# Performance work log

Hardware: AMD Instinct MI355X
Metric: run time of the kernel (lower is better)

The kernel has to match this reference:

```python
import jax, jax.numpy as jnp
import numpy as np

N = 100000   # nodes
E = 1600000  # edges (before self loops)
IN, HID, HEADS, OUT = 128, 32, 2, 32


def setup_inputs() -> dict:
    key = jax.random.key(0)
    ks = jax.random.split(key, 10)
    def glorot(k, shape, fan_in):
        return jax.random.normal(k, shape, dtype=jnp.float32) / np.sqrt(fan_in)
    return {
        "x": jax.random.normal(ks[0], (N, IN), dtype=jnp.float32),
        "edge_index": jax.random.randint(ks[1], (2, E), 0, N, dtype=jnp.int32),
        "W1": glorot(ks[2], (IN, HEADS * HID), IN),
        "a_src1": glorot(ks[3], (HEADS, HID), HID),
        "a_dst1": glorot(ks[4], (HEADS, HID), HID),
        "b1": jnp.zeros((HEADS * HID,), dtype=jnp.float32),
        "W2": glorot(ks[5], (HEADS * HID, OUT), HEADS * HID),
        "a_src2": glorot(ks[6], (1, OUT), OUT),
        "a_dst2": glorot(ks[7], (1, OUT), OUT),
        "b2": jnp.zeros((OUT,), dtype=jnp.float32),
    }


def gat_conv(x, W, a_src, a_dst, b, src, dst, n):
    """PyG-style GATConv: shared linear, edge softmax over incoming edges, sum aggregate."""
    H, C = a_src.shape
    xl = (x @ W).reshape(n, H, C)                       # [N, H, C]
    asn = jnp.einsum('nhc,hc->nh', xl, a_src)            # per-node source score
    adn = jnp.einsum('nhc,hc->nh', xl, a_dst)            # per-node dest score
    e = jax.nn.leaky_relu(asn[src] + adn[dst], 0.2)      # [E', H]
    m = jax.ops.segment_max(e, dst, num_segments=n)      # stable softmax per dest
    m = jnp.where(jnp.isfinite(m), m, 0.0)
    ex = jnp.exp(e - m[dst])
    denom = jax.ops.segment_sum(ex, dst, num_segments=n)
    alpha = ex / (denom[dst] + 1e-16)                    # [E', H]
    out = jax.ops.segment_sum(xl[src] * alpha[:, :, None], dst, num_segments=n)
    return out.reshape(n, H * C) + b


def reference(x, edge_index, W1, a_src1, a_dst1, b1, W2, a_src2, a_dst2, b2):
    n = x.shape[0]
    loop = jnp.arange(n, dtype=edge_index.dtype)         # add self loops (PyG default)
    src = jnp.concatenate([edge_index[0], loop])
    dst = jnp.concatenate([edge_index[1], loop])
    h = jax.nn.relu(gat_conv(x, W1, a_src1, a_dst1, b1, src, dst, n))
    # F.dropout(p=0.5) is identity in eval mode
    return gat_conv(h, W2, a_src2, a_dst2, b2, src, dst, n)
```

## Files before the change

### kernel.cpp

```cpp
#include <hip/hip_runtime.h>
#include <hip/hip_fp16.h>


#define BS 256
#define NB 256
#define PCHUNK 2048
#define CAPB 8192
#define CAP 12000

typedef _Float16 half8 __attribute__((ext_vector_type(8)));
typedef float f32x4 __attribute__((ext_vector_type(4)));

__device__ __forceinline__ int bucket_of(int d, int n) {
    return (d << 8) / n;
}

__global__ __launch_bounds__(BS) void k_init(int* __restrict__ gcursor) {
    gcursor[threadIdx.x] = (int)threadIdx.x * CAPB;
}

__global__ __launch_bounds__(BS) void k_part(const int* __restrict__ ei, int E, int n,
                                             int* __restrict__ gcursor, int* __restrict__ ppair) {
    __shared__ int cnt[NB];
    __shared__ int gpos[NB];
    __shared__ int lcur[NB];
    int t = threadIdx.x;
    cnt[t] = 0; lcur[t] = 0;
    __syncthreads();
    const int* dstp = ei + E;
    int base = blockIdx.x * PCHUNK;
    int pA[PCHUNK / BS], bA[PCHUNK / BS];
#pragma unroll
    for (int k = 0; k < PCHUNK / BS; k++) {
        int idx = base + k * BS + t;
        if (idx < E) {
            int s = ei[idx];
            int d = dstp[idx];
            int b = bucket_of(d, n);
            int lo = (b * n + NB - 1) >> 8;
            bA[k] = b;
            pA[k] = ((d - lo) << 17) | s;
            atomicAdd(&cnt[b], 1);
        } else bA[k] = -1;
    }
    __syncthreads();
    if (cnt[t] > 0) gpos[t] = atomicAdd(&gcursor[t], cnt[t]);
    __syncthreads();
#pragma unroll
    for (int k = 0; k < PCHUNK / BS; k++) {
        if (bA[k] >= 0) {
            int r = atomicAdd(&lcur[bA[k]], 1);
            ppair[gpos[bA[k]] + r] = pA[k];
        }
    }
}

__global__ __launch_bounds__(BS) void k_bucket(const int* __restrict__ ppair,
                                               const int* __restrict__ gcursor, int n,
                                               int* __restrict__ col,
                                               int* __restrict__ row_ptr, int* __restrict__ row_end) {
    __shared__ int ldeg[512];
    __shared__ int lscan[512];
    __shared__ int lcur[512];
    __shared__ int lcol[CAP];
    int b = blockIdx.x;
    int t = threadIdx.x;
    int lo = (b * n + NB - 1) >> 8;
    int hi = ((b + 1) * n + NB - 1) >> 8;
    int W = hi - lo;
    int base = b * CAPB;
    int cnt = gcursor[b] - base;
    if (cnt > CAPB) cnt = CAPB;
    ldeg[t] = 0; ldeg[t + 256] = 0;
    __syncthreads();
    for (int i = t; i < cnt; i += BS) {
        int dlo = ppair[base + i] >> 17;
        atomicAdd(&ldeg[dlo], 1);
    }
    __syncthreads();
    lscan[t] = ldeg[t]; lscan[t + 256] = ldeg[t + 256];
    __syncthreads();
    for (int off = 1; off < 512; off <<= 1) {
        int a0 = (t >= off) ? lscan[t - off] : 0;
        int a1 = (t + 256 >= off) ? lscan[t + 256 - off] : 0;
        __syncthreads();
        lscan[t] += a0; lscan[t + 256] += a1;
        __syncthreads();
    }
    {
        int e0 = lscan[t] - ldeg[t];
        int e1 = lscan[t + 256] - ldeg[t + 256];
        lcur[t] = e0; lcur[t + 256] = e1;
        if (t < W)       { row_ptr[lo + t] = base + e0;       row_end[lo + t] = base + e0 + ldeg[t]; }
        int u = t + 256;
        if (u < W)       { row_ptr[lo + u] = base + e1;       row_end[lo + u] = base + e1 + ldeg[u]; }
    }
    __syncthreads();
    for (int i = t; i < cnt; i += BS) {
        int p = ppair[base + i];
        int r = atomicAdd(&lcur[p >> 17], 1);
        int s = p & 131071;
        if (r < CAP) lcol[r] = s;
        else col[base + r] = s;
    }
    __syncthreads();
    int cmin = cnt < CAP ? cnt : CAP;
    for (int i = t; i < cmin; i += BS) col[base + i] = lcol[i];
}

__global__ __launch_bounds__(BS) void k_gemm1(const float* __restrict__ x, const float* __restrict__ W,
                                              const float* __restrict__ asrc, const float* __restrict__ adst,
                                              __half* __restrict__ xl, float* __restrict__ sc, int n) {
    __shared__ _Float16 wf[16 * 64 * 8];
    int tid = threadIdx.x;
    for (int i = tid; i < 8192; i += BS) {
        int j = i & 7, ln = (i >> 3) & 63, f = i >> 9;
        int kt = f >> 2, nt = f & 3;
        int k = kt * 32 + (ln >> 4) * 8 + j;
        wf[i] = (_Float16)W[k * 64 + nt * 16 + (ln & 15)];
    }
    __syncthreads();
    int wave = tid >> 6, lane = tid & 63;
    int nb = (blockIdx.x * 4 + wave) * 16;
    int m = lane & 15, q = lane >> 4;
    int node_m = nb + m; if (node_m >= n) node_m = n - 1;
    half8 bf[4][4];
#pragma unroll
    for (int f = 0; f < 16; f++)
        bf[f >> 2][f & 3] = *(half8*)&wf[(f * 64 + lane) * 8];
    f32x4 acc[4] = {f32x4{0,0,0,0}, f32x4{0,0,0,0}, f32x4{0,0,0,0}, f32x4{0,0,0,0}};
#pragma unroll
    for (int kt = 0; kt < 4; kt++) {
        const float* xp = x + (size_t)node_m * 128 + kt * 32 + q * 8;
        float4 xa = *(const float4*)xp;
        float4 xb = *(const float4*)(xp + 4);
        half8 a;
        a[0] = (_Float16)xa.x; a[1] = (_Float16)xa.y; a[2] = (_Float16)xa.z; a[3] = (_Float16)xa.w;
        a[4] = (_Float16)xb.x; a[5] = (_Float16)xb.y; a[6] = (_Float16)xb.z; a[7] = (_Float16)xb.w;
#pragma unroll
        for (int nt = 0; nt < 4; nt++)
            acc[nt] = __builtin_amdgcn_mfma_f32_16x16x32_f16(a, bf[kt][nt], acc[nt], 0, 0, 0);
    }
    int c = lane & 15;
    float a_s[4], a_d[4];
#pragma unroll
    for (int nt = 0; nt < 4; nt++) { a_s[nt] = asrc[nt * 16 + c]; a_d[nt] = adst[nt * 16 + c]; }
#pragma unroll
    for (int r = 0; r < 4; r++) {
        int node = nb + q * 4 + r;
        bool ok = node < n;
        float v0 = acc[0][r], v1 = acc[1][r], v2 = acc[2][r], v3 = acc[3][r];
        float as0 = v0 * a_s[0] + v1 * a_s[1];
        float as1 = v2 * a_s[2] + v3 * a_s[3];
        float ad0 = v0 * a_d[0] + v1 * a_d[1];
        float ad1 = v2 * a_d[2] + v3 * a_d[3];
#pragma unroll
        for (int off = 1; off < 16; off <<= 1) {
            as0 += __shfl_xor(as0, off); as1 += __shfl_xor(as1, off);
            ad0 += __shfl_xor(ad0, off); ad1 += __shfl_xor(ad1, off);
        }
        if (ok) {
            __half* row = xl + (size_t)node * 64;
            row[c]      = __float2half(v0);
            row[16 + c] = __float2half(v1);
            row[32 + c] = __float2half(v2);
            row[48 + c] = __float2half(v3);
            if (c == 0) ((float4*)sc)[node] = make_float4(as0, as1, ad0, ad1);
        }
    }
}

__global__ __launch_bounds__(BS) void k_agg1(const int* __restrict__ row_ptr, const int* __restrict__ row_end,
                                             const int* __restrict__ col, const __half* __restrict__ xl,
                                             const float* __restrict__ sc, const float* __restrict__ asrc,
                                             const float* __restrict__ b1,
                                             __half* __restrict__ hout, int n) {
    int tid = blockIdx.x * BS + threadIdx.x;
    int node = tid >> 3;
    int tc = threadIdx.x & 7;
    int lane = threadIdx.x & 63;
    int tb = lane & 56;
    bool alive = node < n;
    if (!alive) node = n - 1;
    float4 acA = ((const float4*)asrc)[tc * 2];
    float4 acB = ((const float4*)asrc)[tc * 2 + 1];
    int s0 = row_ptr[node], e1 = row_end[node];
    float4 sn = ((const float4*)sc)[node];
    bool hh0 = tc < 4;
    float adn = hh0 ? sn.z : sn.w;
    float es0 = sn.x + sn.z; es0 = fmaxf(es0, 0.2f * es0);
    float es1 = sn.y + sn.w; es1 = fmaxf(es1, 0.2f * es1);
    float xs = __expf(hh0 ? es0 : es1);
    uint4 rawS = *(const uint4*)(xl + (size_t)node * 64 + tc * 8);
    __half2 sh0 = *(__half2*)&rawS.x, sh1 = *(__half2*)&rawS.y;
    __half2 sh2 = *(__half2*)&rawS.z, sh3 = *(__half2*)&rawS.w;
    float acc0 = xs * __low2float(sh0), acc1 = xs * __high2float(sh0);
    float acc2 = xs * __low2float(sh1), acc3 = xs * __high2float(sh1);
    float acc4 = xs * __low2float(sh2), acc5 = xs * __high2float(sh2);
    float acc6 = xs * __low2float(sh3), acc7 = xs * __high2float(sh3);
    float den = xs;
    int deg = e1 - s0;
    int mx = deg;
    mx = max(mx, __shfl_xor(mx, 8));
    mx = max(mx, __shfl_xor(mx, 16));
    mx = max(mx, __shfl_xor(mx, 32));
    int nch = (mx + 7) >> 3;
    for (int ci = 0; ci < nch; ci++) {
        int pos = s0 + ci * 8;
        int m = e1 - pos; m = m < 0 ? 0 : (m > 8 ? 8 : m);
        int srcv = (tc < m) ? col[pos + tc] : 0;
#pragma unroll
        for (int k = 0; k < 8; k++) {
            if (k < m) {
                int sE = __shfl(srcv, tb + k);
                uint4 r = *(const uint4*)(xl + (size_t)sE * 64 + tc * 8);
                __half2 q0 = *(__half2*)&r.x, q1 = *(__half2*)&r.y;
                __half2 q2 = *(__half2*)&r.z, q3 = *(__half2*)&r.w;
                float f0 = __low2float(q0), f1 = __high2float(q0);
                float f2 = __low2float(q1), f3 = __high2float(q1);
                float f4 = __low2float(q2), f5 = __high2float(q2);
                float f6 = __low2float(q3), f7 = __high2float(q3);
                float dot = f0 * acA.x + f1 * acA.y + f2 * acA.z + f3 * acA.w
                          + f4 * acB.x + f5 * acB.y + f6 * acB.z + f7 * acB.w;
                dot += __shfl_xor(dot, 1);
                dot += __shfl_xor(dot, 2);
                float e = dot + adn; e = fmaxf(e, 0.2f * e);
                float w = __expf(e);
                acc0 = fmaf(w, f0, acc0); acc1 = fmaf(w, f1, acc1);
                acc2 = fmaf(w, f2, acc2); acc3 = fmaf(w, f3, acc3);
                acc4 = fmaf(w, f4, acc4); acc5 = fmaf(w, f5, acc5);
                acc6 = fmaf(w, f6, acc6); acc7 = fmaf(w, f7, acc7);
                den += w;
            }
        }
    }
    float dinv = 1.f / (den + 1e-16f);
    if (alive) {
        float4 bvA = ((const float4*)b1)[tc * 2];
        float4 bvB = ((const float4*)b1)[tc * 2 + 1];
        __half2 p0 = __floats2half2_rn(fmaxf(fmaf(acc0, dinv, bvA.x), 0.f),
                                       fmaxf(fmaf(acc1, dinv, bvA.y), 0.f));
        __half2 p1 = __floats2half2_rn(fmaxf(fmaf(acc2, dinv, bvA.z), 0.f),
                                       fmaxf(fmaf(acc3, dinv, bvA.w), 0.f));
        __half2 p2 = __floats2half2_rn(fmaxf(fmaf(acc4, dinv, bvB.x), 0.f),
                                       fmaxf(fmaf(acc5, dinv, bvB.y), 0.f));
        __half2 p3 = __floats2half2_rn(fmaxf(fmaf(acc6, dinv, bvB.z), 0.f),
                                       fmaxf(fmaf(acc7, dinv, bvB.w), 0.f));
        uint4 o;
        o.x = *(unsigned int*)&p0; o.y = *(unsigned int*)&p1;
        o.z = *(unsigned int*)&p2; o.w = *(unsigned int*)&p3;
        ((uint4*)(hout + (size_t)node * 64))[tc] = o;
    }
}

__global__ __launch_bounds__(BS) void k_gemm2(const __half* __restrict__ h, const float* __restrict__ W,
                                              const float* __restrict__ asrc, const float* __restrict__ adst,
                                              __half* __restrict__ xl, float* __restrict__ sc, int n) {
    __shared__ _Float16 wf[4 * 64 * 8];
    int tid = threadIdx.x;
    for (int i = tid; i < 2048; i += BS) {
        int j = i & 7, ln = (i >> 3) & 63, f = i >> 9;
        int kt = f >> 1, nt = f & 1;
        int k = kt * 32 + (ln >> 4) * 8 + j;
        wf[i] = (_Float16)W[k * 32 + nt * 16 + (ln & 15)];
    }
    __syncthreads();
    int wave = tid >> 6, lane = tid & 63;
    int nb = (blockIdx.x * 4 + wave) * 16;
    int m = lane & 15, q = lane >> 4;
    int node_m = nb + m; if (node_m >= n) node_m = n - 1;
    half8 bf[2][2];
#pragma unroll
    for (int f = 0; f < 4; f++)
        bf[f >> 1][f & 1] = *(half8*)&wf[(f * 64 + lane) * 8];
    f32x4 acc[2] = {f32x4{0,0,0,0}, f32x4{0,0,0,0}};
#pragma unroll
    for (int kt = 0; kt < 2; kt++) {
        half8 a = *(const half8*)(h + (size_t)node_m * 64 + kt * 32 + q * 8);
#pragma unroll
        for (int nt = 0; nt < 2; nt++)
            acc[nt] = __builtin_amdgcn_mfma_f32_16x16x32_f16(a, bf[kt][nt], acc[nt], 0, 0, 0);
    }
    int c = lane & 15;
    float a_s[2], a_d[2];
#pragma unroll
    for (int nt = 0; nt < 2; nt++) { a_s[nt] = asrc[nt * 16 + c]; a_d[nt] = adst[nt * 16 + c]; }
#pragma unroll
    for (int r = 0; r < 4; r++) {
        int node = nb + q * 4 + r;
        bool ok = node < n;
        float v0 = acc[0][r], v1 = acc[1][r];
        float as = v0 * a_s[0] + v1 * a_s[1];
        float ad = v0 * a_d[0] + v1 * a_d[1];
#pragma unroll
        for (int off = 1; off < 16; off <<= 1) {
            as += __shfl_xor(as, off); ad += __shfl_xor(ad, off);
        }
        if (ok) {
            __half* row = xl + (size_t)node * 32;
            row[c]      = __float2half(v0);
            row[16 + c] = __float2half(v1);
            if (c == 0) ((float2*)sc)[node] = make_float2(as, ad);
        }
    }
}

__global__ __launch_bounds__(BS) void k_agg2(const int* __restrict__ row_ptr, const int* __restrict__ row_end,
                                             const int* __restrict__ col, const __half* __restrict__ xl,
                                             const float* __restrict__ sc, const float* __restrict__ asrc,
                                             const float* __restrict__ b2,
                                             float* __restrict__ out, int n) {
    int tid = blockIdx.x * BS + threadIdx.x;
    int node = tid >> 2;
    int tc = threadIdx.x & 3;
    int lane = threadIdx.x & 63;
    int tb = lane & 60;
    bool alive = node < n;
    if (!alive) node = n - 1;
    float4 acA = ((const float4*)asrc)[tc * 2];
    float4 acB = ((const float4*)asrc)[tc * 2 + 1];
    int s0 = row_ptr[node], e1 = row_end[node];
    float2 sn = ((const float2*)sc)[node];
    float adn = sn.y;
    float es = sn.x + adn; es = fmaxf(es, 0.2f * es);
    float xs = __expf(es);
    uint4 rawS = *(const uint4*)(xl + (size_t)node * 32 + tc * 8);
    __half2 sh0 = *(__half2*)&rawS.x, sh1 = *(__half2*)&rawS.y;
    __half2 sh2 = *(__half2*)&rawS.z, sh3 = *(__half2*)&rawS.w;
    float acc0 = xs * __low2float(sh0), acc1 = xs * __high2float(sh0);
    float acc2 = xs * __low2float(sh1), acc3 = xs * __high2float(sh1);
    float acc4 = xs * __low2float(sh2), acc5 = xs * __high2float(sh2);
    float acc6 = xs * __low2float(sh3), acc7 = xs * __high2float(sh3);
    float den = xs;
    int deg = e1 - s0;
    int mx = deg;
    mx = max(mx, __shfl_xor(mx, 4));
    mx = max(mx, __shfl_xor(mx, 8));
    mx = max(mx, __shfl_xor(mx, 16));
    mx = max(mx, __shfl_xor(mx, 32));
    int nch = (mx + 3) >> 2;
    for (int ci = 0; ci < nch; ci++) {
        int pos = s0 + ci * 4;
        int m = e1 - pos; m = m < 0 ? 0 : (m > 4 ? 4 : m);
        int srcv = (tc < m) ? col[pos + tc] : 0;
#pragma unroll
        for (int k = 0; k < 4; k++) {
            if (k < m) {
                int sE = __shfl(srcv, tb + k);
                uint4 r = *(const uint4*)(xl + (size_t)sE * 32 + tc * 8);
                __half2 q0 = *(__half2*)&r.x, q1 = *(__half2*)&r.y;
                __half2 q2 = *(__half2*)&r.z, q3 = *(__half2*)&r.w;
                float f0 = __low2float(q0), f1 = __high2float(q0);
                float f2 = __low2float(q1), f3 = __high2float(q1);
                float f4 = __low2float(q2), f5 = __high2float(q2);
                float f6 = __low2float(q3), f7 = __high2float(q3);
                float dot = f0 * acA.x + f1 * acA.y + f2 * acA.z + f3 * acA.w
                          + f4 * acB.x + f5 * acB.y + f6 * acB.z + f7 * acB.w;
                dot += __shfl_xor(dot, 1);
                dot += __shfl_xor(dot, 2);
                float e = dot + adn; e = fmaxf(e, 0.2f * e);
                float w = __expf(e);
                acc0 = fmaf(w, f0, acc0); acc1 = fmaf(w, f1, acc1);
                acc2 = fmaf(w, f2, acc2); acc3 = fmaf(w, f3, acc3);
                acc4 = fmaf(w, f4, acc4); acc5 = fmaf(w, f5, acc5);
                acc6 = fmaf(w, f6, acc6); acc7 = fmaf(w, f7, acc7);
                den += w;
            }
        }
    }
    float dinv = 1.f / (den + 1e-16f);
    if (alive) {
        float4 bvA = ((const float4*)b2)[tc * 2];
        float4 bvB = ((const float4*)b2)[tc * 2 + 1];
        float4 oA, oB;
        oA.x = fmaf(acc0, dinv, bvA.x);
        oA.y = fmaf(acc1, dinv, bvA.y);
        oA.z = fmaf(acc2, dinv, bvA.z);
        oA.w = fmaf(acc3, dinv, bvA.w);
        oB.x = fmaf(acc4, dinv, bvB.x);
        oB.y = fmaf(acc5, dinv, bvB.y);
        oB.z = fmaf(acc6, dinv, bvB.z);
        oB.w = fmaf(acc7, dinv, bvB.w);
        float4* orow = (float4*)(out + (size_t)node * 32);
        orow[tc * 2]     = oA;
        orow[tc * 2 + 1] = oB;
    }
}

extern "C" void kernel_launch(void* const* d_in, const int* in_sizes, int n_in,
                              void* d_out, int out_size, void* d_ws, size_t ws_size,
                              hipStream_t stream) {
    const float* x    = (const float*)d_in[0];
    const int*   ei   = (const int*)d_in[1];
    const float* W1   = (const float*)d_in[2];
    const float* as1  = (const float*)d_in[3];
    const float* ad1  = (const float*)d_in[4];
    const float* b1   = (const float*)d_in[5];
    const float* W2   = (const float*)d_in[6];
    const float* as2  = (const float*)d_in[7];
    const float* ad2  = (const float*)d_in[8];
    const float* b2   = (const float*)d_in[9];
    int n = in_sizes[0] / 128;
    int E = in_sizes[1] / 2;

    char* w = (char*)d_ws;
    auto alloc = [&](size_t bytes) -> char* {
        char* p = w; w += (bytes + 255) / 256 * 256; return p;
    };
    int*    gcursor = (int*)alloc(NB * 4);
    int*    ppair   = (int*)alloc((size_t)NB * CAPB * 4);
    int*    col     = (int*)alloc((size_t)NB * CAPB * 4);
    int*    row_ptr = (int*)alloc((size_t)n * 4);
    int*    row_end = (int*)alloc((size_t)n * 4);
    __half* xl1     = (__half*)alloc((size_t)n * 64 * 2);
    float*  sc1     = (float*)alloc((size_t)n * 4 * 4);
    __half* h       = (__half*)alloc((size_t)n * 64 * 2);
    __half* xl2 = xl1;
    float*  sc2 = sc1;

    int gG  = (n + 63) / 64;
    int gA1 = (n * 8 + BS - 1) / BS;
    int gA2 = (n * 4 + BS - 1) / BS;
    int gC  = (E + PCHUNK - 1) / PCHUNK;

    k_init   <<<1, BS, 0, stream>>>(gcursor);
    k_part   <<<gC, BS, 0, stream>>>(ei, E, n, gcursor, ppair);
    k_bucket <<<NB, BS, 0, stream>>>(ppair, gcursor, n, col, row_ptr, row_end);
    k_gemm1  <<<gG, BS, 0, stream>>>(x, W1, as1, ad1, xl1, sc1, n);
    k_agg1   <<<gA1, BS, 0, stream>>>(row_ptr, row_end, col, xl1, sc1, as1, b1, h, n);
    k_gemm2  <<<gG, BS, 0, stream>>>(h, W2, as2, ad2, xl2, sc2, n);
    k_agg2   <<<gA2, BS, 0, stream>>>(row_ptr, row_end, col, xl2, sc2, as2, b2, (float*)d_out, n);
}
```

Before: 241.4 us.

## Fuse edge partition with layer-1 GEMM and aggregation-1 with layer-2 GEMM

Edge partitioning and the layer-1 GEMM are merged into one launch: the first gC blocks partition edges, and the remaining blocks run the GEMM, so the two independent stages can overlap. The layer-1 aggregation kernel now writes its ReLU output into shared memory, and two waves of the same block immediately run the layer-2 MFMA GEMM on it. This removes the global round trip of h and two kernel launches. In exchange, the aggregation kernel uses more LDS and has an extra barrier with half the waves idle during the GEMM, and xl2/sc2 get separate buffers.

```diff
diff --git a/kernel.cpp b/kernel.cpp
--- a/kernel.cpp
+++ b/kernel.cpp
@@ -19,38 +19,101 @@
     gcursor[threadIdx.x] = (int)threadIdx.x * CAPB;
 }
 
-__global__ __launch_bounds__(BS) void k_part(const int* __restrict__ ei, int E, int n,
-                                             int* __restrict__ gcursor, int* __restrict__ ppair) {
-    __shared__ int cnt[NB];
-    __shared__ int gpos[NB];
-    __shared__ int lcur[NB];
-    int t = threadIdx.x;
-    cnt[t] = 0; lcur[t] = 0;
-    __syncthreads();
-    const int* dstp = ei + E;
-    int base = blockIdx.x * PCHUNK;
-    int pA[PCHUNK / BS], bA[PCHUNK / BS];
-#pragma unroll
-    for (int k = 0; k < PCHUNK / BS; k++) {
-        int idx = base + k * BS + t;
-        if (idx < E) {
-            int s = ei[idx];
-            int d = dstp[idx];
-            int b = bucket_of(d, n);
-            int lo = (b * n + NB - 1) >> 8;
-            bA[k] = b;
-            pA[k] = ((d - lo) << 17) | s;
-            atomicAdd(&cnt[b], 1);
-        } else bA[k] = -1;
-    }
-    __syncthreads();
-    if (cnt[t] > 0) gpos[t] = atomicAdd(&gcursor[t], cnt[t]);
-    __syncthreads();
-#pragma unroll
-    for (int k = 0; k < PCHUNK / BS; k++) {
-        if (bA[k] >= 0) {
-            int r = atomicAdd(&lcur[bA[k]], 1);
-            ppair[gpos[bA[k]] + r] = pA[k];
+__global__ __launch_bounds__(BS) void k_pg1(const int* __restrict__ ei, int E, int n,
+                                            int* __restrict__ gcursor, int* __restrict__ ppair,
+                                            const float* __restrict__ x, const float* __restrict__ W,
+                                            const float* __restrict__ asrc, const float* __restrict__ adst,
+                                            __half* __restrict__ xl, float* __restrict__ sc, int gC) {
+    __shared__ _Float16 smem[8192];
+    int tid = threadIdx.x;
+    if ((int)blockIdx.x < gC) {
+        int* cnt  = (int*)smem;
+        int* gpos = cnt + NB;
+        int* lcur = cnt + 2 * NB;
+        cnt[tid] = 0; lcur[tid] = 0;
+        __syncthreads();
+        const int* dstp = ei + E;
+        int base = blockIdx.x * PCHUNK;
+        int pA[PCHUNK / BS], bA[PCHUNK / BS];
+#pragma unroll
+        for (int k = 0; k < PCHUNK / BS; k++) {
+            int idx = base + k * BS + tid;
+            if (idx < E) {
+                int s = ei[idx];
+                int d = dstp[idx];
+                int b = bucket_of(d, n);
+                int lo = (b * n + NB - 1) >> 8;
+                bA[k] = b;
+                pA[k] = ((d - lo) << 17) | s;
+                atomicAdd(&cnt[b], 1);
+            } else bA[k] = -1;
+        }
+        __syncthreads();
+        if (cnt[tid] > 0) gpos[tid] = atomicAdd(&gcursor[tid], cnt[tid]);
+        __syncthreads();
+#pragma unroll
+        for (int k = 0; k < PCHUNK / BS; k++) {
+            if (bA[k] >= 0) {
+                int r = atomicAdd(&lcur[bA[k]], 1);
+                ppair[gpos[bA[k]] + r] = pA[k];
+            }
+        }
+        return;
+    }
+    _Float16* wf = smem;
+    for (int i = tid; i < 8192; i += BS) {
+        int j = i & 7, ln = (i >> 3) & 63, f = i >> 9;
+        int kt = f >> 2, nt = f & 3;
+        int k = kt * 32 + (ln >> 4) * 8 + j;
+        wf[i] = (_Float16)W[k * 64 + nt * 16 + (ln & 15)];
+    }
+    __syncthreads();
+    int wave = tid >> 6, lane = tid & 63;
+    int nb = ((blockIdx.x - gC) * 4 + wave) * 16;
+    int m = lane & 15, q = lane >> 4;
+    int node_m = nb + m; if (node_m >= n) node_m = n - 1;
+    half8 bf[4][4];
+#pragma unroll
+    for (int f = 0; f < 16; f++)
+        bf[f >> 2][f & 3] = *(half8*)&wf[(f * 64 + lane) * 8];
+    f32x4 acc[4] = {f32x4{0,0,0,0}, f32x4{0,0,0,0}, f32x4{0,0,0,0}, f32x4{0,0,0,0}};
+#pragma unroll
+    for (int kt = 0; kt < 4; kt++) {
+        const float* xp = x + (size_t)node_m * 128 + kt * 32 + q * 8;
+        float4 xa = *(const float4*)xp;
+        float4 xb = *(const float4*)(xp + 4);
+        half8 a;
+        a[0] = (_Float16)xa.x; a[1] = (_Float16)xa.y; a[2] = (_Float16)xa.z; a[3] = (_Float16)xa.w;
+        a[4] = (_Float16)xb.x; a[5] = (_Float16)xb.y; a[6] = (_Float16)xb.z; a[7] = (_Float16)xb.w;
+#pragma unroll
+        for (int nt = 0; nt < 4; nt++)
+            acc[nt] = __builtin_amdgcn_mfma_f32_16x16x32_f16(a, bf[kt][nt], acc[nt], 0, 0, 0);
+    }
+    int c = lane & 15;
+    float a_s[4], a_d[4];
+#pragma unroll
+    for (int nt = 0; nt < 4; nt++) { a_s[nt] = asrc[nt * 16 + c]; a_d[nt] = adst[nt * 16 + c]; }
+#pragma unroll
+    for (int r = 0; r < 4; r++) {
+        int node = nb + q * 4 + r;
+        bool ok = node < n;
+        float v0 = acc[0][r], v1 = acc[1][r], v2 = acc[2][r], v3 = acc[3][r];
+        float as0 = v0 * a_s[0] + v1 * a_s[1];
+        float as1 = v2 * a_s[2] + v3 * a_s[3];
+        float ad0 = v0 * a_d[0] + v1 * a_d[1];
+        float ad1 = v2 * a_d[2] + v3 * a_d[3];
+#pragma unroll
+        for (int off = 1; off < 16; off <<= 1) {
+            as0 += __shfl_xor(as0, off); as1 += __shfl_xor(as1, off);
+            ad0 += __shfl_xor(ad0, off); ad1 += __shfl_xor(ad1, off);
+        }
+        if (ok) {
+            __half* row = xl + (size_t)node * 64;
+            row[c]      = __float2half(v0);
+            row[16 + c] = __float2half(v1);
+            row[32 + c] = __float2half(v2);
+            row[48 + c] = __float2half(v3);
+            if (c == 0) ((float4*)sc)[node] = make_float4(as0, as1, ad0, ad1);
         }
     }
 }
@@ -108,90 +171,39 @@
     for (int i = t; i < cmin; i += BS) col[base + i] = lcol[i];
 }
 
-__global__ __launch_bounds__(BS) void k_gemm1(const float* __restrict__ x, const float* __restrict__ W,
-                                              const float* __restrict__ asrc, const float* __restrict__ adst,
-                                              __half* __restrict__ xl, float* __restrict__ sc, int n) {
-    __shared__ _Float16 wf[16 * 64 * 8];
+__global__ __launch_bounds__(BS) void k_ag1g2(const int* __restrict__ row_ptr, const int* __restrict__ row_end,
+                                              const int* __restrict__ col, const __half* __restrict__ xl,
+                                              const float* __restrict__ sc, const float* __restrict__ asrc,
+                                              const float* __restrict__ b1,
+                                              const float* __restrict__ W2,
+                                              const float* __restrict__ as2, const float* __restrict__ ad2,
+                                              __half* __restrict__ xl2, float* __restrict__ sc2, int n) {
+    __shared__ _Float16 hsh[32 * 72];
+    __shared__ _Float16 wf2[2048];
     int tid = threadIdx.x;
-    for (int i = tid; i < 8192; i += BS) {
+    for (int i = tid; i < 2048; i += BS) {
         int j = i & 7, ln = (i >> 3) & 63, f = i >> 9;
-        int kt = f >> 2, nt = f & 3;
+        int kt = f >> 1, nt = f & 1;
         int k = kt * 32 + (ln >> 4) * 8 + j;
-        wf[i] = (_Float16)W[k * 64 + nt * 16 + (ln & 15)];
-    }
-    __syncthreads();
-    int wave = tid >> 6, lane = tid & 63;
-    int nb = (blockIdx.x * 4 + wave) * 16;
-    int m = lane & 15, q = lane >> 4;
-    int node_m = nb + m; if (node_m >= n) node_m = n - 1;
-    half8 bf[4][4];
-#pragma unroll
-    for (int f = 0; f < 16; f++)
-        bf[f >> 2][f & 3] = *(half8*)&wf[(f * 64 + lane) * 8];
-    f32x4 acc[4] = {f32x4{0,0,0,0}, f32x4{0,0,0,0}, f32x4{0,0,0,0}, f32x4{0,0,0,0}};
-#pragma unroll
-    for (int kt = 0; kt < 4; kt++) {
-        const float* xp = x + (size_t)node_m * 128 + kt * 32 + q * 8;
-        float4 xa = *(const float4*)xp;
-        float4 xb = *(const float4*)(xp + 4);
-        half8 a;
-        a[0] = (_Float16)xa.x; a[1] = (_Float16)xa.y; a[2] = (_Float16)xa.z; a[3] = (_Float16)xa.w;
-        a[4] = (_Float16)xb.x; a[5] = (_Float16)xb.y; a[6] = (_Float16)xb.z; a[7] = (_Float16)xb.w;
-#pragma unroll
-        for (int nt = 0; nt < 4; nt++)
-            acc[nt] = __builtin_amdgcn_mfma_f32_16x16x32_f16(a, bf[kt][nt], acc[nt], 0, 0, 0);
-    }
-    int c = lane & 15;
-    float a_s[4], a_d[4];
-#pragma unroll
-    for (int nt = 0; nt < 4; nt++) { a_s[nt] = asrc[nt * 16 + c]; a_d[nt] = adst[nt * 16 + c]; }
-#pragma unroll
-    for (int r = 0; r < 4; r++) {
-        int node = nb + q * 4 + r;
-        bool ok = node < n;
-        float v0 = acc[0][r], v1 = acc[1][r], v2 = acc[2][r], v3 = acc[3][r];
-        float as0 = v0 * a_s[0] + v1 * a_s[1];
-        float as1 = v2 * a_s[2] + v3 * a_s[3];
-        float ad0 = v0 * a_d[0] + v1 * a_d[1];
-        float ad1 = v2 * a_d[2] + v3 * a_d[3];
-#pragma unroll
-        for (int off = 1; off < 16; off <<= 1) {
-            as0 += __shfl_xor(as0, off); as1 += __shfl_xor(as1, off);
-            ad0 += __shfl_xor(ad0, off); ad1 += __shfl_xor(ad1, off);
-        }
-        if (ok) {
-            __half* row = xl + (size_t)node * 64;
-            row[c]      = __float2half(v0);
-            row[16 + c] = __float2half(v1);
-            row[32 + c] = __float2half(v2);
-            row[48 + c] = __float2half(v3);
-            if (c == 0) ((float4*)sc)[node] = make_float4(as0, as1, ad0, ad1);
-        }
-    }
-}
-
-__global__ __launch_bounds__(BS) void k_agg1(const int* __restrict__ row_ptr, const int* __restrict__ row_end,
-                                             const int* __restrict__ col, const __half* __restrict__ xl,
-                                             const float* __restrict__ sc, const float* __restrict__ asrc,
-                                             const float* __restrict__ b1,
-                                             __half* __restrict__ hout, int n) {
-    int tid = blockIdx.x * BS + threadIdx.x;
-    int node = tid >> 3;
-    int tc = threadIdx.x & 7;
-    int lane = threadIdx.x & 63;
+        wf2[i] = (_Float16)W2[k * 32 + nt * 16 + (ln & 15)];
+    }
+    int node_local = tid >> 3;
+    int node = blockIdx.x * 32 + node_local;
+    int tc = tid & 7;
+    int lane = tid & 63;
     int tb = lane & 56;
     bool alive = node < n;
-    if (!alive) node = n - 1;
+    int nodeC = alive ? node : n - 1;
     float4 acA = ((const float4*)asrc)[tc * 2];
     float4 acB = ((const float4*)asrc)[tc * 2 + 1];
-    int s0 = row_ptr[node], e1 = row_end[node];
-    float4 sn = ((const float4*)sc)[node];
+    int s0 = row_ptr[nodeC], e1 = row_end[nodeC];
+    float4 sn = ((const float4*)sc)[nodeC];
     bool hh0 = tc < 4;
     float adn = hh0 ? sn.z : sn.w;
     float es0 = sn.x + sn.z; es0 = fmaxf(es0, 0.2f * es0);
     float es1 = sn.y + sn.w; es1 = fmaxf(es1, 0.2f * es1);
     float xs = __expf(hh0 ? es0 : es1);
-    uint4 rawS = *(const uint4*)(xl + (size_t)node * 64 + tc * 8);
+    uint4 rawS = *(const uint4*)(xl + (size_t)nodeC * 64 + tc * 8);
     __half2 sh0 = *(__half2*)&rawS.x, sh1 = *(__half2*)&rawS.y;
     __half2 sh2 = *(__half2*)&rawS.z, sh3 = *(__half2*)&rawS.w;
     float acc0 = xs * __low2float(sh0), acc1 = xs * __high2float(sh0);
@@ -235,7 +247,7 @@
         }
     }
     float dinv = 1.f / (den + 1e-16f);
-    if (alive) {
+    {
         float4 bvA = ((const float4*)b1)[tc * 2];
         float4 bvB = ((const float4*)b1)[tc * 2 + 1];
         __half2 p0 = __floats2half2_rn(fmaxf(fmaf(acc0, dinv, bvA.x), 0.f),
@@ -249,58 +261,47 @@
         uint4 o;
         o.x = *(unsigned int*)&p0; o.y = *(unsigned int*)&p1;
         o.z = *(unsigned int*)&p2; o.w = *(unsigned int*)&p3;
-        ((uint4*)(hout + (size_t)node * 64))[tc] = o;
-    }
-}
-
-__global__ __launch_bounds__(BS) void k_gemm2(const __half* __restrict__ h, const float* __restrict__ W,
-                                              const float* __restrict__ asrc, const float* __restrict__ adst,
-                                              __half* __restrict__ xl, float* __restrict__ sc, int n) {
-    __shared__ _Float16 wf[4 * 64 * 8];
-    int tid = threadIdx.x;
-    for (int i = tid; i < 2048; i += BS) {
-        int j = i & 7, ln = (i >> 3) & 63, f = i >> 9;
-        int kt = f >> 1, nt = f & 1;
-        int k = kt * 32 + (ln >> 4) * 8 + j;
-        wf[i] = (_Float16)W[k * 32 + nt * 16 + (ln & 15)];
-    }
-    __syncthreads();
-    int wave = tid >> 6, lane = tid & 63;
-    int nb = (blockIdx.x * 4 + wave) * 16;
-    int m = lane & 15, q = lane >> 4;
-    int node_m = nb + m; if (node_m >= n) node_m = n - 1;
-    half8 bf[2][2];
-#pragma unroll
-    for (int f = 0; f < 4; f++)
-        bf[f >> 1][f & 1] = *(half8*)&wf[(f * 64 + lane) * 8];
-    f32x4 acc[2] = {f32x4{0,0,0,0}, f32x4{0,0,0,0}};
-#pragma unroll
-    for (int kt = 0; kt < 2; kt++) {
-        half8 a = *(const half8*)(h + (size_t)node_m * 64 + kt * 32 + q * 8);
-#pragma unroll
-        for (int nt = 0; nt < 2; nt++)
-            acc[nt] = __builtin_amdgcn_mfma_f32_16x16x32_f16(a, bf[kt][nt], acc[nt], 0, 0, 0);
-    }
-    int c = lane & 15;
-    float a_s[2], a_d[2];
-#pragma unroll
-    for (int nt = 0; nt < 2; nt++) { a_s[nt] = asrc[nt * 16 + c]; a_d[nt] = adst[nt * 16 + c]; }
-#pragma unroll
-    for (int r = 0; r < 4; r++) {
-        int node = nb + q * 4 + r;
-        bool ok = node < n;
-        float v0 = acc[0][r], v1 = acc[1][r];
-        float as = v0 * a_s[0] + v1 * a_s[1];
-        float ad = v0 * a_d[0] + v1 * a_d[1];
-#pragma unroll
-        for (int off = 1; off < 16; off <<= 1) {
-            as += __shfl_xor(as, off); ad += __shfl_xor(ad, off);
-        }
-        if (ok) {
-            __half* row = xl + (size_t)node * 32;
-            row[c]      = __float2half(v0);
-            row[16 + c] = __float2half(v1);
-            if (c == 0) ((float2*)sc)[node] = make_float2(as, ad);
+        *(uint4*)&hsh[node_local * 72 + tc * 8] = o;
+    }
+    __syncthreads();
+    int wave = tid >> 6;
+    if (wave < 2) {
+        int m2 = lane & 15, q2 = lane >> 4;
+        int nl = wave * 16 + m2;
+        half8 bf[2][2];
+#pragma unroll
+        for (int f = 0; f < 4; f++)
+            bf[f >> 1][f & 1] = *(half8*)&wf2[(f * 64 + lane) * 8];
+        f32x4 acc2g[2] = {f32x4{0,0,0,0}, f32x4{0,0,0,0}};
+#pragma unroll
+        for (int kt = 0; kt < 2; kt++) {
+            half8 a = *(half8*)&hsh[nl * 72 + kt * 32 + q2 * 8];
+#pragma unroll
+            for (int nt = 0; nt < 2; nt++)
+                acc2g[nt] = __builtin_amdgcn_mfma_f32_16x16x32_f16(a, bf[kt][nt], acc2g[nt], 0, 0, 0);
+        }
+        int c = lane & 15;
+        float a_s[2], a_d[2];
+#pragma unroll
+        for (int nt = 0; nt < 2; nt++) { a_s[nt] = as2[nt * 16 + c]; a_d[nt] = ad2[nt * 16 + c]; }
+#pragma unroll
+        for (int r = 0; r < 4; r++) {
+            int nl_r = wave * 16 + q2 * 4 + r;
+            int node_r = blockIdx.x * 32 + nl_r;
+            bool ok = node_r < n;
+            float v0 = acc2g[0][r], v1 = acc2g[1][r];
+            float as = v0 * a_s[0] + v1 * a_s[1];
+            float ad = v0 * a_d[0] + v1 * a_d[1];
+#pragma unroll
+            for (int off = 1; off < 16; off <<= 1) {
+                as += __shfl_xor(as, off); ad += __shfl_xor(ad, off);
+            }
+            if (ok) {
+                __half* row = xl2 + (size_t)node_r * 32;
+                row[c]      = __float2half(v0);
+                row[16 + c] = __float2half(v1);
+                if (c == 0) ((float2*)sc2)[node_r] = make_float2(as, ad);
+            }
         }
     }
 }
@@ -414,20 +415,20 @@
     int*    row_end = (int*)alloc((size_t)n * 4);
     __half* xl1     = (__half*)alloc((size_t)n * 64 * 2);
     float*  sc1     = (float*)alloc((size_t)n * 4 * 4);
-    __half* h       = (__half*)alloc((size_t)n * 64 * 2);
-    __half* xl2 = xl1;
-    float*  sc2 = sc1;
-
+    __half* xl2     = (__half*)alloc((size_t)n * 32 * 2);
+    float*  sc2     = (float*)alloc((size_t)n * 2 * 4);
+
+    int gC  = (E + PCHUNK - 1) / PCHUNK;
     int gG  = (n + 63) / 64;
     int gA1 = (n * 8 + BS - 1) / BS;
     int gA2 = (n * 4 + BS - 1) / BS;
-    int gC  = (E + PCHUNK - 1) / PCHUNK;
 
     k_init   <<<1, BS, 0, stream>>>(gcursor);
-    k_part   <<<gC, BS, 0, stream>>>(ei, E, n, gcursor, ppair);
+    k_pg1    <<<gC + gG, BS, 0, stream>>>(ei, E, n, gcursor, ppair,
+                                          x, W1, as1, ad1, xl1, sc1, gC);
     k_bucket <<<NB, BS, 0, stream>>>(ppair, gcursor, n, col, row_ptr, row_end);
-    k_gemm1  <<<gG, BS, 0, stream>>>(x, W1, as1, ad1, xl1, sc1, n);
-    k_agg1   <<<gA1, BS, 0, stream>>>(row_ptr, row_end, col, xl1, sc1, as1, b1, h, n);
-    k_gemm2  <<<gG, BS, 0, stream>>>(h, W2, as2, ad2, xl2, sc2, n);
-    k_agg2   <<<gA2, BS, 0, stream>>>(row_ptr, row_end, col, xl2, sc2, as2, b2, (float*)d_out, n);
-}
+    k_ag1g2  <<<gA1, BS, 0, stream>>>(row_ptr, row_end, col, xl1, sc1, as1, b1,
+                                      W2, as2, ad2, xl2, sc2, n);
+    k_agg2   <<<gA2, BS, 0, stream>>>(row_ptr, row_end, col, xl2, sc2, as2, b2,
+                                      (float*)d_out, n);
+}
```

Result: faster. 230.7 us (-4.4%).
